# Kernel optimization log

Hardware: AMD Instinct MI355X
Metric: run time of the kernel (lower is better)

## Reference

```python
import jax, jax.numpy as jnp
import numpy as np

# Geometry hardcoded by the torch module
B = 512        # added batch dim (SpykeTorch processes one sample; we vectorize)
T = 30         # timesteps (spike-wave dim 0)
H = 41         # 8*4 + 9 rows so that 9 sections of height 9 tile with stride 4
WF = 40        # frequency bands == kernel width
NSEC = 9       # n_conv_sections
SECLEN = 4     # n_section_length (also conv output height per section: 9-6+1=4)
NF = 50        # n_feature_maps
KH = 6         # kernel height
THRESH = 23.0  # sf.fire threshold


def setup_inputs() -> dict:
    key = jax.random.key(0)
    k1, k2 = jax.random.split(key)
    # binary spike-wave input (cumulative spike tensors are {0,1})
    x = jax.random.randint(k1, (B, T, 1, H, WF), 0, 2).astype(jnp.float32)
    # 9 independent convs, each [out=50, in=1, 6, 40], N(0.8, 0.05) init
    W = 0.8 + 0.05 * jax.random.normal(k2, (NSEC, NF, 1, KH, WF), dtype=jnp.float32)
    return {"x": x, "W": W}


def _conv_section(xs, w):
    # xs: [B*T, 1, 9, 40], w: [50, 1, 6, 40] -> [B*T, 50, 4, 1] (valid conv, no bias)
    return jax.lax.conv_general_dilated(
        xs, w, window_strides=(1, 1), padding="VALID",
        dimension_numbers=("NCHW", "OIHW", "NCHW"))


def _compute_pots(x, W):
    # Returns per-section conv potentials, stacked: [NSEC, B, T, NF, SECLEN]
    Bn, Tn = x.shape[0], x.shape[1]
    xf = x.reshape(Bn * Tn, 1, H, WF)
    pots = []
    for i in range(NSEC):  # fixed small structural loop (distinct weights per section)
        xs = xf[:, :, i * SECLEN: i * SECLEN + KH + SECLEN - 1, :]  # rows [i*4, i*4+9)
        pot = _conv_section(xs, W[i]).reshape(Bn, Tn, NF, SECLEN)   # width collapses to 1
        pots.append(pot)
    return jnp.stack(pots)


def _winners_from_pot(pot):
    # pot: [B, T, NF, SECLEN] raw conv potentials for one section.
    # sf.fire: spike where potential >= threshold
    spk = (pot >= THRESH).astype(pot.dtype)
    # snn.Pooling((4,40)) on a [T,50,4,1] map == global spatial max -> [B, T, NF]
    pooled = spk.max(axis=3)
    # sf.get_k_winners(pooled, kwta=1, inhibition_radius=0):
    s = pooled  # pooled potentials are binary, so sign(p) == p
    Tn = pot.shape[1]
    # earliest-spike timestep per (batch, feature); clamp like torch .clamp_(0, T-1)
    first = jnp.clip(Tn - s.sum(axis=1), 0, Tn - 1).astype(jnp.int32)   # [B, NF]
    vals = jnp.take_along_axis(s, first[:, None, :], axis=1)[:, 0, :]   # [B, NF]
    trunc = s * vals[:, None, :]                                        # [B, T, NF]
    v = trunc.max(axis=(1, 2)) * Tn                                     # prioritize early spikes
    trunc = trunc + s * v[:, None, None]
    total = trunc.sum(axis=1)                                           # [B, NF]
    win = jnp.where(total.max(axis=1) > 0,
                    jnp.argmax(total, axis=1).astype(jnp.int32),
                    jnp.int32(-1))                                      # -1 == empty winners
    return win


def reference(x, W):
    pots = _compute_pots(x, W)                       # [NSEC, B, T, NF, SECLEN]
    winners = jax.vmap(_winners_from_pot)(pots)      # [NSEC, B] winner feature or -1
    return winners, pots
```

## Files before the change

### kernel.cpp

```cpp
#include <hip/hip_runtime.h>

#define BB 512
#define TT 30
#define HH 41
#define WFW 40
#define NSEC 9
#define SECLEN 4
#define NF 50
#define KH 6
#define THRESH 23.0f
#define NBT (BB*TT)
#define WIN_CNT (NSEC*BB)
#define NT_HALF 15
#define ROWF (HH*WFW)
#define SLAB_B 3360
#define XBYTES (NT_HALF*SLAB_B)
#define WSW_BYTES (NSEC*4*8*64*16)
#define MASK_BYTES (NSEC*BB*2*64*4)

typedef __attribute__((ext_vector_type(8))) short short8;
typedef __attribute__((ext_vector_type(4))) float f32x4;

__global__ __launch_bounds__(256) void wconv_kernel(const float* __restrict__ W,
                                                    unsigned char* __restrict__ wsw)
{
    int gid  = blockIdx.x * 256 + threadIdx.x;
    int frag = gid >> 6, l = gid & 63;
    int i    = frag >> 5, rem = frag & 31;
    int nt   = rem >> 3,  kc  = rem & 7;
    int f    = nt * 16 + (l & 15);
    int kb   = kc * 32 + (l >> 4) * 8;
    unsigned d0 = 0, d1 = 0, d2 = 0, d3 = 0;
    if (f < NF && kb < KH * WFW) {
        const float* src = W + (size_t)(i * NF + f) * (KH * WFW) + kb;
        float4 v0 = ((const float4*)src)[0];
        float4 v1 = ((const float4*)src)[1];
        float vv[8] = {v0.x, v0.y, v0.z, v0.w, v1.x, v1.y, v1.z, v1.w};
        unsigned r[8];
        #pragma unroll
        for (int j = 0; j < 8; ++j) {
            unsigned a = __float_as_uint(vv[j]);
            r[j] = (a + 0x7FFFu + ((a >> 16) & 1u)) >> 16;
        }
        d0 = r[0] | (r[1] << 16); d1 = r[2] | (r[3] << 16);
        d2 = r[4] | (r[5] << 16); d3 = r[6] | (r[7] << 16);
    }
    ((uint4*)wsw)[gid] = make_uint4(d0, d1, d2, d3);
}

template<bool WRITE_MASK>
__global__ __launch_bounds__(256, 3) void pots_mfma(const float* __restrict__ x,
                                                    const unsigned char* __restrict__ wsw,
                                                    float* __restrict__ out,
                                                    unsigned* __restrict__ msk)
{
    __shared__ alignas(16) unsigned char xs[XBYTES];
    __shared__ unsigned long long wsc[NSEC * 4 * 4];
    const int tid = threadIdx.x;
    const int blk = blockIdx.x;
    const int b   = blk >> 1, h = blk & 1;
    const int bt0 = b * TT + h * NT_HALF;

    const float* xg = x + (size_t)bt0 * ROWF;
    #pragma unroll
    for (int it = 0; it < 25; ++it) {
        int idx = tid + it * 256;
        if (idx < NT_HALF * 410) {
            int r = idx / 410, pos = idx - r * 410;
            const float4 v = *(const float4*)(xg + (size_t)r * ROWF + pos * 4);
            unsigned u0 = __float_as_uint(v.x), u1 = __float_as_uint(v.y);
            unsigned u2 = __float_as_uint(v.z), u3 = __float_as_uint(v.w);
            uint2 p;
            p.x = (u0 >> 16) | (u1 & 0xFFFF0000u);
            p.y = (u2 >> 16) | (u3 & 0xFFFF0000u);
            *(uint2*)(xs + r * SLAB_B + pos * 8) = p;
        }
    }
    if (tid < 150) {
        int r = tid / 10, part = tid - r * 10;
        *(uint2*)(xs + r * SLAB_B + 3280 + part * 8) = make_uint2(0, 0);
    }
    __syncthreads();

    const int l   = tid & 63, nt = tid >> 6;
    const int q   = l >> 4;
    const int f16 = l & 15;
    const int ff  = nt * 16 + f16;

    unsigned ab[4];
    #pragma unroll
    for (int Mt = 0; Mt < 4; ++Mt) {
        int m = Mt * 16 + (l & 15); if (m > 59) m = 59;
        ab[Mt] = (unsigned)(m >> 2) * SLAB_B + (unsigned)(m & 3) * 80 + (unsigned)q * 16;
    }
    const unsigned char* wb = wsw + (size_t)nt * 8192 + (size_t)l * 16;

    short8 bf[2][8];
    #pragma unroll
    for (int kc = 0; kc < 8; ++kc)
        bf[0][kc] = *(const short8*)(wb + kc * 1024);

    #pragma unroll
    for (int i = 0; i < NSEC; ++i) {
        const int cur = i & 1, nxt = cur ^ 1;
        if (i < NSEC - 1) {
            const unsigned char* wbn = wb + (size_t)(i + 1) * 32768;
            #pragma unroll
            for (int kc = 0; kc < 8; ++kc)
                bf[nxt][kc] = *(const short8*)(wbn + kc * 1024);
        }

        f32x4 acc[4];
        #pragma unroll
        for (int Mt = 0; Mt < 4; ++Mt) acc[Mt] = (f32x4){0.f, 0.f, 0.f, 0.f};

        const unsigned ib = (unsigned)i * 320;
        #pragma unroll
        for (int kc = 0; kc < 8; ++kc) {
            #pragma unroll
            for (int Mt = 0; Mt < 4; ++Mt) {
                short8 a = *(const short8*)(xs + ab[Mt] + ib + kc * 64);
                acc[Mt] = __builtin_amdgcn_mfma_f32_16x16x32_bf16(a, bf[cur][kc], acc[Mt], 0, 0, 0);
            }
        }

        #pragma unroll
        for (int Mt = 0; Mt < 4; ++Mt) {
            const int t_loc = Mt * 4 + q;
            float m2 = fmaxf(fmaxf(acc[Mt][0], acc[Mt][1]),
                             fmaxf(acc[Mt][2], acc[Mt][3]));
            unsigned long long bal = __ballot(m2 >= THRESH);
            if (WRITE_MASK && l == 0) wsc[(i * 4 + nt) * 4 + Mt] = bal;
            if (t_loc < NT_HALF && ff < NF) {
                size_t o = ((size_t)i * NBT + bt0 + t_loc) * NF + ff;
                *(float4*)(out + WIN_CNT + o * 4) =
                    make_float4(acc[Mt][0], acc[Mt][1], acc[Mt][2], acc[Mt][3]);
            }
        }
    }

    if (WRITE_MASK) {
        __syncthreads();
        #pragma unroll
        for (int it = 0; it < 3; ++it) {
            int idx = tid + it * 256;
            if (idx < NSEC * 64) {
                int i  = idx >> 6, f = idx & 63;
                int ng = f >> 4,  fl = f & 15;
                unsigned m = 0;
                #pragma unroll
                for (int Mt = 0; Mt < 4; ++Mt) {
                    unsigned long long w =
                        (wsc[(i * 4 + ng) * 4 + Mt] >> fl) & 0x0001000100010001ULL;
                    unsigned bq = (unsigned)((w | (w >> 15) | (w >> 30) | (w >> 45)) & 0xFULL);
                    m |= bq << (Mt * 4);
                }
                m &= 0x7FFFu;
                msk[((size_t)(i * BB + b) * 2 + h) * 64 + f] = m;
            }
        }
    }
}

__global__ __launch_bounds__(256) void win_msk(const unsigned* __restrict__ msk,
                                               float* __restrict__ out)
{
    const int sub = threadIdx.x >> 6;
    const int f   = threadIdx.x & 63;
    const int blk = blockIdx.x * 4 + sub;
    unsigned m0 = msk[(size_t)blk * 128 + f];
    unsigned m1 = msk[(size_t)blk * 128 + 64 + f];
    unsigned mask = m0 | (m1 << 15);
    int c     = __popc(mask);
    int first = TT - c; if (first > TT - 1) first = TT - 1;
    int fv    = (f < NF) ? (int)((mask >> first) & 1u) : 0;
    unsigned long long bal = __ballot(fv != 0);
    int v30 = (bal != 0ull) ? TT : 0;
    int tot = (f < NF) ? c * (fv + v30) : -1;
    int idx = f;
    for (int off = 32; off > 0; off >>= 1) {
        int ot = __shfl_xor(tot, off);
        int oi = __shfl_xor(idx, off);
        if (ot > tot || (ot == tot && oi < idx)) { tot = ot; idx = oi; }
    }
    if (f == 0) out[blk] = (float)((tot > 0) ? idx : -1);
}

__global__ __launch_bounds__(64) void win_pots(float* __restrict__ out)
{
    const int blk = blockIdx.x;
    const int f   = threadIdx.x;
    const float* po = out + WIN_CNT + (size_t)blk * TT * NF * SECLEN;
    unsigned mask = 0u;
    if (f < NF) {
        for (int t = 0; t < TT; ++t) {
            const float4 v = *(const float4*)(po + ((size_t)t * NF + f) * SECLEN);
            float m = fmaxf(fmaxf(v.x, v.y), fmaxf(v.z, v.w));
            if (m >= THRESH) mask |= (1u << t);
        }
    }
    int c     = __popc(mask);
    int first = TT - c; if (first > TT - 1) first = TT - 1;
    int fv    = (f < NF) ? (int)((mask >> first) & 1u) : 0;
    unsigned long long bal = __ballot(fv != 0);
    int v30 = (bal != 0ull) ? TT : 0;
    int tot = (f < NF) ? c * (fv + v30) : -1;
    int idx = f;
    for (int off = 32; off > 0; off >>= 1) {
        int ot = __shfl_xor(tot, off);
        int oi = __shfl_xor(idx, off);
        if (ot > tot || (ot == tot && oi < idx)) { tot = ot; idx = oi; }
    }
    if (f == 0) out[blk] = (float)((tot > 0) ? idx : -1);
}

extern "C" void kernel_launch(void* const* d_in, const int* in_sizes, int n_in,
                              void* d_out, int out_size, void* d_ws, size_t ws_size,
                              hipStream_t stream)
{
    const float* x = (const float*)d_in[0];
    const float* W = (const float*)d_in[1];
    float* out = (float*)d_out;
    unsigned char* wsw = (unsigned char*)d_ws;
    unsigned* msk = (unsigned*)(wsw + WSW_BYTES);
    const bool use_msk = ws_size >= (size_t)(WSW_BYTES + MASK_BYTES);

    wconv_kernel<<<(NSEC*4*8*64) / 256, 256, 0, stream>>>(W, wsw);
    if (use_msk) {
        pots_mfma<true><<<BB * 2, 256, 0, stream>>>(x, wsw, out, msk);
        win_msk<<<(NSEC * BB) / 4, 256, 0, stream>>>(msk, out);
    } else {
        pots_mfma<false><<<BB * 2, 256, 0, stream>>>(x, wsw, out, nullptr);
        win_pots<<<NSEC * BB, 64, 0, stream>>>(out);
    }
}
```

Measured before the change: 52.70 us.

## Pre-pack binary spike input into bitmasks before the MFMA conv kernel

```diff
diff --git a/kernel.cpp b/kernel.cpp
--- a/kernel.cpp
+++ b/kernel.cpp
@@ -15,11 +15,42 @@
 #define ROWF (HH*WFW)
 #define SLAB_B 3360
 #define XBYTES (NT_HALF*SLAB_B)
+#define PKW 52
 #define WSW_BYTES (NSEC*4*8*64*16)
 #define MASK_BYTES (NSEC*BB*2*64*4)
+#define XPK_BYTES (NBT*PKW*4)
 
 typedef __attribute__((ext_vector_type(8))) short short8;
 typedef __attribute__((ext_vector_type(4))) float f32x4;
+
+__global__ __launch_bounds__(256) void xpack_kernel(const float* __restrict__ x,
+                                                    unsigned* __restrict__ xpk)
+{
+    int gid = blockIdx.x * 256 + threadIdx.x;
+    int row = gid / PKW, wi = gid - row * PKW;
+    const float* src = x + (size_t)row * ROWF + wi * 32;
+    unsigned bits = 0;
+    if (wi < PKW - 1) {
+        #pragma unroll
+        for (int j4 = 0; j4 < 8; ++j4) {
+            float4 v = ((const float4*)src)[j4];
+            bits |= (v.x != 0.f ? 1u : 0u) << (4*j4+0);
+            bits |= (v.y != 0.f ? 1u : 0u) << (4*j4+1);
+            bits |= (v.z != 0.f ? 1u : 0u) << (4*j4+2);
+            bits |= (v.w != 0.f ? 1u : 0u) << (4*j4+3);
+        }
+    } else {
+        #pragma unroll
+        for (int j4 = 0; j4 < 2; ++j4) {
+            float4 v = ((const float4*)src)[j4];
+            bits |= (v.x != 0.f ? 1u : 0u) << (4*j4+0);
+            bits |= (v.y != 0.f ? 1u : 0u) << (4*j4+1);
+            bits |= (v.z != 0.f ? 1u : 0u) << (4*j4+2);
+            bits |= (v.w != 0.f ? 1u : 0u) << (4*j4+3);
+        }
+    }
+    xpk[gid] = bits;
+}
 
 __global__ __launch_bounds__(256) void wconv_kernel(const float* __restrict__ W,
                                                     unsigned char* __restrict__ wsw)
@@ -48,11 +79,12 @@
     ((uint4*)wsw)[gid] = make_uint4(d0, d1, d2, d3);
 }
 
-template<bool WRITE_MASK>
+template<bool WRITE_MASK, bool FROM_BITS>
 __global__ __launch_bounds__(256, 3) void pots_mfma(const float* __restrict__ x,
                                                     const unsigned char* __restrict__ wsw,
                                                     float* __restrict__ out,
-                                                    unsigned* __restrict__ msk)
+                                                    unsigned* __restrict__ msk,
+                                                    const unsigned* __restrict__ xpk)
 {
     __shared__ alignas(16) unsigned char xs[XBYTES];
     __shared__ unsigned long long wsc[NSEC * 4 * 4];
@@ -61,24 +93,53 @@
     const int b   = blk >> 1, h = blk & 1;
     const int bt0 = b * TT + h * NT_HALF;
 
-    const float* xg = x + (size_t)bt0 * ROWF;
-    #pragma unroll
-    for (int it = 0; it < 25; ++it) {
-        int idx = tid + it * 256;
-        if (idx < NT_HALF * 410) {
-            int r = idx / 410, pos = idx - r * 410;
-            const float4 v = *(const float4*)(xg + (size_t)r * ROWF + pos * 4);
-            unsigned u0 = __float_as_uint(v.x), u1 = __float_as_uint(v.y);
-            unsigned u2 = __float_as_uint(v.z), u3 = __float_as_uint(v.w);
-            uint2 p;
-            p.x = (u0 >> 16) | (u1 & 0xFFFF0000u);
-            p.y = (u2 >> 16) | (u3 & 0xFFFF0000u);
-            *(uint2*)(xs + r * SLAB_B + pos * 8) = p;
-        }
-    }
-    if (tid < 150) {
-        int r = tid / 10, part = tid - r * 10;
-        *(uint2*)(xs + r * SLAB_B + 3280 + part * 8) = make_uint2(0, 0);
+    if (FROM_BITS) {
+        const unsigned* pkr = xpk + (size_t)bt0 * PKW;
+        #pragma unroll
+        for (int it = 0; it < 4; ++it) {
+            int g = tid + it * 256;
+            if (g < NT_HALF * PKW) {
+                int r = g / PKW, wi = g - r * PKW;
+                unsigned w = pkr[g];
+                unsigned char* dst = xs + r * SLAB_B + wi * 64;
+                #pragma unroll
+                for (int j = 0; j < 4; ++j) {
+                    unsigned o0 = (((w >> (8*j+0)) & 1u) ? 0x3F80u : 0u)
+                                | (((w >> (8*j+1)) & 1u) ? 0x3F800000u : 0u);
+                    unsigned o1 = (((w >> (8*j+2)) & 1u) ? 0x3F80u : 0u)
+                                | (((w >> (8*j+3)) & 1u) ? 0x3F800000u : 0u);
+                    unsigned o2 = (((w >> (8*j+4)) & 1u) ? 0x3F80u : 0u)
+                                | (((w >> (8*j+5)) & 1u) ? 0x3F800000u : 0u);
+                    unsigned o3 = (((w >> (8*j+6)) & 1u) ? 0x3F80u : 0u)
+                                | (((w >> (8*j+7)) & 1u) ? 0x3F800000u : 0u);
+                    *(uint4*)(dst + j * 16) = make_uint4(o0, o1, o2, o3);
+                }
+            }
+        }
+        if (tid < 60) {
+            int r = tid >> 2, part = tid & 3;
+            *(uint2*)(xs + r * SLAB_B + 3328 + part * 8) = make_uint2(0, 0);
+        }
+    } else {
+        const float* xg = x + (size_t)bt0 * ROWF;
+        #pragma unroll
+        for (int it = 0; it < 25; ++it) {
+            int idx = tid + it * 256;
+            if (idx < NT_HALF * 410) {
+                int r = idx / 410, pos = idx - r * 410;
+                const float4 v = *(const float4*)(xg + (size_t)r * ROWF + pos * 4);
+                unsigned u0 = __float_as_uint(v.x), u1 = __float_as_uint(v.y);
+                unsigned u2 = __float_as_uint(v.z), u3 = __float_as_uint(v.w);
+                uint2 p;
+                p.x = (u0 >> 16) | (u1 & 0xFFFF0000u);
+                p.y = (u2 >> 16) | (u3 & 0xFFFF0000u);
+                *(uint2*)(xs + r * SLAB_B + pos * 8) = p;
+            }
+        }
+        if (tid < 150) {
+            int r = tid / 10, part = tid - r * 10;
+            *(uint2*)(xs + r * SLAB_B + 3280 + part * 8) = make_uint2(0, 0);
+        }
     }
     __syncthreads();
 
@@ -223,14 +284,18 @@
     float* out = (float*)d_out;
     unsigned char* wsw = (unsigned char*)d_ws;
     unsigned* msk = (unsigned*)(wsw + WSW_BYTES);
-    const bool use_msk = ws_size >= (size_t)(WSW_BYTES + MASK_BYTES);
+    unsigned* xpk = (unsigned*)(wsw + WSW_BYTES + MASK_BYTES);
 
     wconv_kernel<<<(NSEC*4*8*64) / 256, 256, 0, stream>>>(W, wsw);
-    if (use_msk) {
-        pots_mfma<true><<<BB * 2, 256, 0, stream>>>(x, wsw, out, msk);
+    if (ws_size >= (size_t)(WSW_BYTES + MASK_BYTES + XPK_BYTES)) {
+        xpack_kernel<<<(NBT * PKW) / 256, 256, 0, stream>>>(x, xpk);
+        pots_mfma<true, true><<<BB * 2, 256, 0, stream>>>(x, wsw, out, msk, xpk);
+        win_msk<<<(NSEC * BB) / 4, 256, 0, stream>>>(msk, out);
+    } else if (ws_size >= (size_t)(WSW_BYTES + MASK_BYTES)) {
+        pots_mfma<true, false><<<BB * 2, 256, 0, stream>>>(x, wsw, out, msk, nullptr);
         win_msk<<<(NSEC * BB) / 4, 256, 0, stream>>>(msk, out);
     } else {
-        pots_mfma<false><<<BB * 2, 256, 0, stream>>>(x, wsw, out, nullptr);
+        pots_mfma<false, false><<<BB * 2, 256, 0, stream>>>(x, wsw, out, nullptr, nullptr);
         win_pots<<<NSEC * BB, 64, 0, stream>>>(out);
     }
 }
```

Result: slower. 62.71 us (+19.0%).
